# Kernel optimization log

Hardware: AMD Instinct MI355X
Metric: run time of the kernel (lower is better)

Reference implementation:

```python
import jax, jax.numpy as jnp
import numpy as np

NEG_SLOPE = 0.2  # PyG GATConv default negative_slope


def _gat(x, src, dst, N, W, a_src, a_dst, b, heads, ch, concat):
    # x: [N, F_in]; src/dst: [E] (self-loops already appended)
    h = (x @ W).reshape(N, heads, ch)                      # [N,H,C]
    s = jnp.sum(h * a_src, axis=-1)                        # [N,H]
    d = jnp.sum(h * a_dst, axis=-1)                        # [N,H]
    e = jax.nn.leaky_relu(s[src] + d[dst], NEG_SLOPE)      # [E,H]
    # segment softmax over incoming edges of each dst node
    m = jax.ops.segment_max(e, dst, num_segments=N)        # [N,H]
    ex = jnp.exp(e - m[dst])
    den = jax.ops.segment_sum(ex, dst, num_segments=N)     # [N,H]
    alpha = ex / den[dst]                                  # [E,H]
    out = jax.ops.segment_sum(h[src] * alpha[:, :, None], dst, num_segments=N)  # [N,H,C]
    out = out.reshape(N, heads * ch) if concat else out.mean(axis=1)
    return out + b


def setup_inputs() -> dict:
    key = jax.random.key(0)
    ks = jax.random.split(key, 20)
    N, E, F_in, H, C = 50000, 400000, 64, 4, 128
    x = jax.random.normal(ks[0], (N, F_in), dtype=jnp.float32)
    edge_index = jax.random.randint(ks[1], (2, E), 0, N, dtype=jnp.int64)

    def lin(k, fi, fo):
        return jax.random.normal(k, (fi, fo), dtype=jnp.float32) / np.float32(np.sqrt(fi))

    def att(k, h, c):
        return jax.random.normal(k, (h, c), dtype=jnp.float32) / np.float32(np.sqrt(c))

    return {
        "x": x, "edge_index": edge_index,
        "W1": lin(ks[2], F_in, H * C), "as1": att(ks[3], H, C), "ad1": att(ks[4], H, C), "b1": jnp.zeros((H * C,), jnp.float32),
        "W2": lin(ks[5], H * C, H * C), "as2": att(ks[6], H, C), "ad2": att(ks[7], H, C), "b2": jnp.zeros((H * C,), jnp.float32),
        "W3": lin(ks[8], H * C, C), "as3": att(ks[9], 1, C), "ad3": att(ks[10], 1, C), "b3": jnp.zeros((C,), jnp.float32),
        "cW1": lin(ks[11], C, C // 2), "cb1": jnp.zeros((C // 2,), jnp.float32),
        "cW2": lin(ks[12], C // 2, 2), "cb2": jnp.zeros((2,), jnp.float32),
    }


def reference(x, edge_index, W1, as1, ad1, b1, W2, as2, ad2, b2, W3, as3, ad3, b3, cW1, cb1, cW2, cb2):
    N = x.shape[0]
    loops = jnp.arange(N, dtype=edge_index.dtype)
    src = jnp.concatenate([edge_index[0], loops])
    dst = jnp.concatenate([edge_index[1], loops])
    h = _gat(x, src, dst, N, W1, as1, ad1, b1, 4, 128, True)
    h = jax.nn.relu(h)                         # dropout is identity at eval
    h = _gat(h, src, dst, N, W2, as2, ad2, b2, 4, 128, True)
    h = jax.nn.relu(h)
    h = _gat(h, src, dst, N, W3, as3, ad3, b3, 1, 128, False)
    out = jax.nn.relu(h @ cW1 + cb1) @ cW2 + cb2
    return jax.nn.log_softmax(out, axis=-1)
```

## Files before the change

kernel.cpp:

```cpp
#include <hip/hip_runtime.h>
#include <math.h>

#define NEG_SLOPE 0.2f

typedef __attribute__((ext_vector_type(8))) short short8;
typedef __attribute__((ext_vector_type(4))) float f32x4;
typedef unsigned short ushort_t;
typedef unsigned int u32;
typedef __attribute__((ext_vector_type(8))) unsigned short ushort8;
typedef __attribute__((ext_vector_type(4))) unsigned short ushort4v;

__device__ inline ushort_t f2bf(float f) {
    unsigned int u = __builtin_bit_cast(unsigned int, f);
    u += 0x7fffu + ((u >> 16) & 1u);
    return (ushort_t)(u >> 16);
}
__device__ inline float bf2f(ushort_t u) {
    unsigned int v = ((unsigned int)u) << 16;
    return __builtin_bit_cast(float, v);
}

__device__ inline void gl_lds16(const ushort_t* g, ushort_t* l) {
    __builtin_amdgcn_global_load_lds((const __attribute__((address_space(1))) u32*)g,
                                     (__attribute__((address_space(3))) u32*)l, 16, 0, 0);
}


__global__ void convert_count_kernel(const int* __restrict__ ei, int E, int N,
                                     int* __restrict__ deg,
                                     const float* __restrict__ x, ushort_t* __restrict__ xb, int n4x,
                                     const float* __restrict__ W1, ushort_t* __restrict__ W1t,
                                     const float* __restrict__ W2, ushort_t* __restrict__ W2t,
                                     const float* __restrict__ W3, ushort_t* __restrict__ W3t,
                                     const float* __restrict__ cW1, ushort_t* __restrict__ cW1t) {
    int i = blockIdx.x * blockDim.x + threadIdx.x;
    if (i < E + N) {
        int d = (i < E) ? ei[E + i] : (i - E);
        atomicAdd(&deg[d], 1);
    }
    if (i < n4x) {
        float4 v = ((const float4*)x)[i];
        ushort4v o;
        o.x = f2bf(v.x); o.y = f2bf(v.y); o.z = f2bf(v.z); o.w = f2bf(v.w);
        ((ushort4v*)xb)[i] = o;
        return;
    }
    int j = i - n4x;
    if (j < 64 * 512) {
        int k = j / 512, nn = j % 512;
        W1t[(size_t)nn * 64 + k] = f2bf(W1[j]);
        return;
    }
    j -= 64 * 512;
    if (j < 512 * 512) {
        int k = j / 512, nn = j % 512;
        W2t[(size_t)nn * 512 + k] = f2bf(W2[j]);
        return;
    }
    j -= 512 * 512;
    if (j < 512 * 128) {
        int k = j / 128, nn = j % 128;
        W3t[(size_t)nn * 512 + k] = f2bf(W3[j]);
        return;
    }
    j -= 512 * 128;
    if (j < 128 * 64) {
        int k = j / 64, nn = j % 64;
        cW1t[(size_t)nn * 128 + k] = f2bf(cW1[j]);
    }
}

__global__ void scan1_kernel(const int* __restrict__ deg, int* __restrict__ rowptr,
                             int* __restrict__ bsum, int N) {
    __shared__ int sdata[256];
    int t = threadIdx.x;
    int base = blockIdx.x * 1024 + t * 4;
    int v[4];
#pragma unroll
    for (int k = 0; k < 4; k++) v[k] = (base + k < N) ? deg[base + k] : 0;
    int s = v[0] + v[1] + v[2] + v[3];
    sdata[t] = s;
    __syncthreads();
    for (int off = 1; off < 256; off <<= 1) {
        int x = (t >= off) ? sdata[t - off] : 0;
        __syncthreads();
        sdata[t] += x;
        __syncthreads();
    }
    int p = sdata[t] - s;
    if (t == 255) bsum[blockIdx.x] = sdata[255];
#pragma unroll
    for (int k = 0; k < 4; k++) {
        if (base + k < N) rowptr[base + k] = p;
        p += v[k];
    }
}

__global__ void scan2_kernel(int* __restrict__ bsum, int* __restrict__ rowptr, int nb, int N) {
    __shared__ int sh[256];
    int t = threadIdx.x;
    int v = (t < nb) ? bsum[t] : 0;
    sh[t] = v;
    __syncthreads();
    for (int off = 1; off < 256; off <<= 1) {
        int x = (t >= off) ? sh[t - off] : 0;
        __syncthreads();
        sh[t] += x;
        __syncthreads();
    }
    if (t < nb) bsum[t] = sh[t] - v;
    if (t == 255) rowptr[N] = sh[255];
}

__global__ void scan3_kernel(const int* __restrict__ bsum, int* __restrict__ rowptr,
                             int* __restrict__ cursor, int N) {
    int i = blockIdx.x * blockDim.x + threadIdx.x;
    if (i < N) {
        int v = rowptr[i] + bsum[i >> 10];
        rowptr[i] = v;
        cursor[i] = v;
    }
}

__global__ void fill_csr_kernel(const int* __restrict__ ei, int E, int N,
                                int* __restrict__ cursor, int* __restrict__ srcS) {
    int e = blockIdx.x * blockDim.x + threadIdx.x;
    if (e >= E + N) return;
    int s, d;
    if (e < E) { s = ei[e]; d = ei[E + e]; }
    else       { s = e - E; d = e - E; }
    int pos = atomicAdd(&cursor[d], 1);
    srcS[pos] = s;
}


template <bool SCORES>
__global__ __launch_bounds__(256, 2) void gemm_bf16_kernel(
    const ushort_t* __restrict__ A, const ushort_t* __restrict__ Bt,
    ushort_t* __restrict__ C,
    const float* __restrict__ a_s, const float* __restrict__ a_d,
    float* __restrict__ sOut, float* __restrict__ dOut, int H,
    int M, int Ncols, int K) {
    __shared__ ushort_t As[128 * 32];
    __shared__ ushort_t Bs[128 * 32];
    __shared__ float sL[2][128];
    __shared__ float dL[2][128];
    int bm = blockIdx.y * 128, bn = blockIdx.x * 128;
    int tid = threadIdx.x;
    int w = tid >> 6, lane = tid & 63;
    int wy = w >> 1, wx = w & 1;
    int r = lane & 15, quad = lane >> 4;
    int srow = lane >> 2;
    int scol = (lane & 3) * 8;
    f32x4 acc[4][4] = {};
    for (int k0 = 0; k0 < K; k0 += 32) {
#pragma unroll
        for (int it = 0; it < 2; it++) {
            int rowb = w * 32 + it * 16;
            gl_lds16(A  + (size_t)(bm + rowb + srow) * K + k0 + scol, As + rowb * 32);
            gl_lds16(Bt + (size_t)(bn + rowb + srow) * K + k0 + scol, Bs + rowb * 32);
        }
        __syncthreads();
        short8 af[4], bfr[4];
#pragma unroll
        for (int i = 0; i < 4; i++)
            af[i] = *(const short8*)(As + (wy * 64 + i * 16 + r) * 32 + quad * 8);
#pragma unroll
        for (int j = 0; j < 4; j++)
            bfr[j] = *(const short8*)(Bs + (wx * 64 + j * 16 + r) * 32 + quad * 8);
#pragma unroll
        for (int i = 0; i < 4; i++)
#pragma unroll
            for (int j = 0; j < 4; j++)
                acc[i][j] = __builtin_amdgcn_mfma_f32_16x16x32_bf16(af[i], bfr[j], acc[i][j], 0, 0, 0);
        __syncthreads();
    }
#pragma unroll
    for (int i = 0; i < 4; i++) {
        int rowb = bm + wy * 64 + i * 16 + quad * 4;
#pragma unroll
        for (int j = 0; j < 4; j++) {
            int col = bn + wx * 64 + j * 16 + r;
            if (col >= Ncols) continue;
#pragma unroll
            for (int reg = 0; reg < 4; reg++) {
                int row = rowb + reg;
                if (row < M) C[(size_t)row * Ncols + col] = f2bf(acc[i][j][reg]);
            }
        }
    }
    if (SCORES) {
        int head = bn >> 7;
        float av[4], bv[4];
#pragma unroll
        for (int j = 0; j < 4; j++) {
            int c = wx * 64 + j * 16 + r;
            av[j] = a_s[head * 128 + c];
            bv[j] = a_d[head * 128 + c];
        }
#pragma unroll
        for (int i = 0; i < 4; i++) {
#pragma unroll
            for (int reg = 0; reg < 4; reg++) {
                float ps = acc[i][0][reg] * av[0] + acc[i][1][reg] * av[1]
                         + acc[i][2][reg] * av[2] + acc[i][3][reg] * av[3];
                float pd = acc[i][0][reg] * bv[0] + acc[i][1][reg] * bv[1]
                         + acc[i][2][reg] * bv[2] + acc[i][3][reg] * bv[3];
#pragma unroll
                for (int off = 8; off >= 1; off >>= 1) {
                    ps += __shfl_down(ps, off, 16);
                    pd += __shfl_down(pd, off, 16);
                }
                if (r == 0) {
                    int row128 = wy * 64 + i * 16 + quad * 4 + reg;
                    sL[wx][row128] = ps;
                    dL[wx][row128] = pd;
                }
            }
        }
        __syncthreads();
        if (tid < 128) {
            int row = bm + tid;
            if (row < M) {
                sOut[(size_t)row * H + head] = sL[0][tid] + sL[1][tid];
                dOut[(size_t)row * H + head] = dL[0][tid] + dL[1][tid];
            }
        }
    }
}


template <int HC, bool RELU>
__global__ void agg_fused_kernel(const ushort_t* __restrict__ h, const float* __restrict__ s,
                                 const float* __restrict__ dv, const int* __restrict__ rowptr,
                                 const int* __restrict__ srcS, const float* __restrict__ bias,
                                 ushort_t* __restrict__ outp, int N, int H) {
    const int TPN = HC / 8;
    const int NPB = 256 / TPN;
    int n = blockIdx.x * NPB + threadIdx.x / TPN;
    int c8 = threadIdx.x % TPN;
    if (n >= N) return;
    int head = (c8 * 8) >> 7;
    int g = c8 & 15;
    float dn = dv[(size_t)n * H + head];
    int beg = rowptr[n], end = rowptr[n + 1];
    float acc0[8] = {0.f, 0.f, 0.f, 0.f, 0.f, 0.f, 0.f, 0.f};
    float acc1[8] = {0.f, 0.f, 0.f, 0.f, 0.f, 0.f, 0.f, 0.f};
    float den = 0.f;
    for (int cb = beg; cb < end; cb += 16) {
        int je = cb + g;
        int svg = 0;
        float al = 0.f;
        if (je < end) {
            svg = srcS[je];
            float e = s[(size_t)svg * H + head] + dn;
            e = (e >= 0.f) ? e : NEG_SLOPE * e;
            al = expf(fminf(e, 80.f));
        }
        int kmax = end - cb;
        if (kmax > 16) kmax = 16;
        int k = 0;
        for (; k + 4 <= kmax; k += 4) {
            float a0 = __shfl(al, k, 16),     a1 = __shfl(al, k + 1, 16);
            float a2 = __shfl(al, k + 2, 16), a3 = __shfl(al, k + 3, 16);
            int s0 = __shfl(svg, k, 16),      s1 = __shfl(svg, k + 1, 16);
            int s2 = __shfl(svg, k + 2, 16),  s3 = __shfl(svg, k + 3, 16);
            den += a0 + a1 + a2 + a3;
            ushort8 hv0 = *(const ushort8*)(h + (size_t)s0 * HC + c8 * 8);
            ushort8 hv1 = *(const ushort8*)(h + (size_t)s1 * HC + c8 * 8);
            ushort8 hv2 = *(const ushort8*)(h + (size_t)s2 * HC + c8 * 8);
            ushort8 hv3 = *(const ushort8*)(h + (size_t)s3 * HC + c8 * 8);
#pragma unroll
            for (int kk = 0; kk < 8; kk++) {
                acc0[kk] += a0 * bf2f(hv0[kk]) + a2 * bf2f(hv2[kk]);
                acc1[kk] += a1 * bf2f(hv1[kk]) + a3 * bf2f(hv3[kk]);
            }
        }
        for (; k < kmax; k++) {
            float a0 = __shfl(al, k, 16);
            int s0 = __shfl(svg, k, 16);
            den += a0;
            ushort8 hv0 = *(const ushort8*)(h + (size_t)s0 * HC + c8 * 8);
#pragma unroll
            for (int kk = 0; kk < 8; kk++) acc0[kk] += a0 * bf2f(hv0[kk]);
        }
    }
    float inv = 1.f / den;
    float4 bv0 = ((const float4*)bias)[c8 * 2];
    float4 bv1 = ((const float4*)bias)[c8 * 2 + 1];
    float r[8];
#pragma unroll
    for (int k = 0; k < 8; k++) r[k] = (acc0[k] + acc1[k]) * inv;
    r[0] += bv0.x; r[1] += bv0.y; r[2] += bv0.z; r[3] += bv0.w;
    r[4] += bv1.x; r[5] += bv1.y; r[6] += bv1.z; r[7] += bv1.w;
    if (RELU) {
#pragma unroll
        for (int k = 0; k < 8; k++) r[k] = fmaxf(r[k], 0.f);
    }
    ushort8 o;
#pragma unroll
    for (int k = 0; k < 8; k++) o[k] = f2bf(r[k]);
    ((ushort8*)outp)[(size_t)n * TPN + c8] = o;
}


__global__ __launch_bounds__(256, 2) void cls_fused_kernel(
    const ushort_t* __restrict__ A, const ushort_t* __restrict__ Bt,
    const float* __restrict__ cb1, const float* __restrict__ cW2,
    const float* __restrict__ cb2, float* __restrict__ out, int M) {
    __shared__ ushort_t As[128 * 32];
    __shared__ ushort_t Bs[128 * 32];
    __shared__ float l0L[128];
    __shared__ float l1L[128];
    int bm = blockIdx.y * 128;
    int tid = threadIdx.x;
    int w = tid >> 6, lane = tid & 63;
    int wy = w >> 1, wx = w & 1;
    int r = lane & 15, quad = lane >> 4;
    int srow = lane >> 2;
    int scol = (lane & 3) * 8;
    const int K = 128;
    f32x4 acc[4][4] = {};
    for (int k0 = 0; k0 < K; k0 += 32) {
#pragma unroll
        for (int it = 0; it < 2; it++) {
            int rowb = w * 32 + it * 16;
            gl_lds16(A  + (size_t)(bm + rowb + srow) * K + k0 + scol, As + rowb * 32);
            gl_lds16(Bt + (size_t)(rowb + srow) * K + k0 + scol, Bs + rowb * 32);
        }
        __syncthreads();
        short8 af[4], bfr[4];
#pragma unroll
        for (int i = 0; i < 4; i++)
            af[i] = *(const short8*)(As + (wy * 64 + i * 16 + r) * 32 + quad * 8);
#pragma unroll
        for (int j = 0; j < 4; j++)
            bfr[j] = *(const short8*)(Bs + (wx * 64 + j * 16 + r) * 32 + quad * 8);
#pragma unroll
        for (int i = 0; i < 4; i++)
#pragma unroll
            for (int j = 0; j < 4; j++)
                acc[i][j] = __builtin_amdgcn_mfma_f32_16x16x32_bf16(af[i], bfr[j], acc[i][j], 0, 0, 0);
        __syncthreads();
    }
    if (wx == 0) {
        float c1v[4], w20[4], w21[4];
#pragma unroll
        for (int j = 0; j < 4; j++) {
            int c = j * 16 + r;
            c1v[j] = cb1[c];
            w20[j] = cW2[c * 2];
            w21[j] = cW2[c * 2 + 1];
        }
#pragma unroll
        for (int i = 0; i < 4; i++) {
#pragma unroll
            for (int reg = 0; reg < 4; reg++) {
                float ps = 0.f, pd = 0.f;
#pragma unroll
                for (int j = 0; j < 4; j++) {
                    float v = fmaxf(acc[i][j][reg] + c1v[j], 0.f);
                    ps += v * w20[j];
                    pd += v * w21[j];
                }
#pragma unroll
                for (int off = 8; off >= 1; off >>= 1) {
                    ps += __shfl_down(ps, off, 16);
                    pd += __shfl_down(pd, off, 16);
                }
                if (r == 0) {
                    int row128 = wy * 64 + i * 16 + quad * 4 + reg;
                    l0L[row128] = ps;
                    l1L[row128] = pd;
                }
            }
        }
    }
    __syncthreads();
    if (tid < 128) {
        int row = bm + tid;
        if (row < M) {
            float l0 = l0L[tid] + cb2[0];
            float l1 = l1L[tid] + cb2[1];
            float mm = fmaxf(l0, l1);
            float lse = mm + logf(expf(l0 - mm) + expf(l1 - mm));
            out[(size_t)row * 2 + 0] = l0 - lse;
            out[(size_t)row * 2 + 1] = l1 - lse;
        }
    }
}


extern "C" void kernel_launch(void* const* d_in, const int* in_sizes, int n_in,
                              void* d_out, int out_size, void* d_ws, size_t ws_size,
                              hipStream_t stream) {
    const float* x   = (const float*)d_in[0];
    const int*   ei  = (const int*)d_in[1];
    const float* W1  = (const float*)d_in[2];
    const float* as1 = (const float*)d_in[3];
    const float* ad1 = (const float*)d_in[4];
    const float* b1  = (const float*)d_in[5];
    const float* W2  = (const float*)d_in[6];
    const float* as2 = (const float*)d_in[7];
    const float* ad2 = (const float*)d_in[8];
    const float* b2  = (const float*)d_in[9];
    const float* W3  = (const float*)d_in[10];
    const float* as3 = (const float*)d_in[11];
    const float* ad3 = (const float*)d_in[12];
    const float* b3  = (const float*)d_in[13];
    const float* cW1 = (const float*)d_in[14];
    const float* cb1 = (const float*)d_in[15];
    const float* cW2 = (const float*)d_in[16];
    const float* cb2 = (const float*)d_in[17];
    float* outp = (float*)d_out;

    const int N  = in_sizes[0] / 64;
    const int E  = in_sizes[1] / 2;
    const int E2 = E + N;
    const int NB = (N + 1023) / 1024;
    const int n4x = N * 16;

    char* ws = (char*)d_ws;
    size_t off = 0;
    auto alloc = [&](size_t bytes) -> void* {
        void* p = ws + off;
        off += (bytes + 255) & ~(size_t)255;
        return p;
    };
    ushort_t* Ab     = (ushort_t*)alloc((size_t)N * 512 * 2);
    ushort_t* Bb     = (ushort_t*)alloc((size_t)N * 512 * 2);
    ushort_t* xb     = (ushort_t*)alloc((size_t)N * 64 * 2);
    ushort_t* W1t    = (ushort_t*)alloc((size_t)512 * 64 * 2);
    ushort_t* W2t    = (ushort_t*)alloc((size_t)512 * 512 * 2);
    ushort_t* W3t    = (ushort_t*)alloc((size_t)128 * 512 * 2);
    ushort_t* cW1t   = (ushort_t*)alloc((size_t)128 * 128 * 2);
    float*    sbuf   = (float*)alloc((size_t)N * 4 * 4);
    float*    dbuf   = (float*)alloc((size_t)N * 4 * 4);
    int*      srcS   = (int*)alloc((size_t)E2 * 4);
    int*      deg    = (int*)alloc((size_t)N * 4);
    int*      cursor = (int*)alloc((size_t)N * 4);
    int*      rowptr = (int*)alloc((size_t)(N + 1) * 4);
    int*      bsum   = (int*)alloc((size_t)256 * 4);
    (void)ws_size; (void)n_in; (void)out_size;

    hipMemsetAsync(deg, 0, (size_t)N * 4, stream);
    {
        int tot = n4x + 64 * 512 + 512 * 512 + 512 * 128 + 128 * 64;
        if (E2 > tot) tot = E2;
        convert_count_kernel<<<(tot + 255) / 256, 256, 0, stream>>>(
            ei, E, N, deg, x, xb, n4x, W1, W1t, W2, W2t, W3, W3t, cW1, cW1t);
    }
    scan1_kernel<<<NB, 256, 0, stream>>>(deg, rowptr, bsum, N);
    scan2_kernel<<<1, 256, 0, stream>>>(bsum, rowptr, NB, N);
    scan3_kernel<<<(N + 255) / 256, 256, 0, stream>>>(bsum, rowptr, cursor, N);
    fill_csr_kernel<<<(E2 + 255) / 256, 256, 0, stream>>>(ei, E, N, cursor, srcS);

    dim3 gB(256);
    dim3 g512(4, (N + 127) / 128);
    dim3 g128(1, (N + 127) / 128);

    gemm_bf16_kernel<true><<<g512, gB, 0, stream>>>(
        xb, W1t, Ab, as1, ad1, sbuf, dbuf, 4, N, 512, 64);
    agg_fused_kernel<512, true><<<(N + 3) / 4, 256, 0, stream>>>(
        Ab, sbuf, dbuf, rowptr, srcS, b1, Bb, N, 4);

    gemm_bf16_kernel<true><<<g512, gB, 0, stream>>>(
        Bb, W2t, Ab, as2, ad2, sbuf, dbuf, 4, N, 512, 512);
    agg_fused_kernel<512, true><<<(N + 3) / 4, 256, 0, stream>>>(
        Ab, sbuf, dbuf, rowptr, srcS, b2, Bb, N, 4);

    gemm_bf16_kernel<true><<<g128, gB, 0, stream>>>(
        Bb, W3t, Ab, as3, ad3, sbuf, dbuf, 1, N, 128, 512);
    agg_fused_kernel<128, false><<<(N + 15) / 16, 256, 0, stream>>>(
        Ab, sbuf, dbuf, rowptr, srcS, b3, Bb, N, 1);

    cls_fused_kernel<<<g128, gB, 0, stream>>>(Bb, cW1t, cb1, cW2, cb2, outp, N);
}
```

Measured before the change: 415.3 us.

## Software-pipeline gather loads and prefetch next edge chunk in GAT aggregation

Restructures the per-node aggregation loop so neighbor feature rows are loaded in double-buffered groups of four before the attention weights are computed. The source index and score for the next 16-edge chunk are prefetched during the current chunk's work. The goal is to hide the dependent-load latency chain (index, then score, then feature row) behind accumulation. In exchange it raises register pressure from eight buffered ushort8 rows plus prefetch state, which could lower occupancy.

```diff
diff --git a/kernel.cpp b/kernel.cpp
--- a/kernel.cpp
+++ b/kernel.cpp
@@ -247,44 +247,160 @@
     float acc0[8] = {0.f, 0.f, 0.f, 0.f, 0.f, 0.f, 0.f, 0.f};
     float acc1[8] = {0.f, 0.f, 0.f, 0.f, 0.f, 0.f, 0.f, 0.f};
     float den = 0.f;
+
+    const ushort_t* hb = h + (size_t)c8 * 8;
+
+    int je = beg + g;
+    int svg = 0;
+    float sv = 0.f;
+    if (je < end) {
+        svg = srcS[je];
+        sv = s[(size_t)svg * H + head];
+    }
+
     for (int cb = beg; cb < end; cb += 16) {
-        int je = cb + g;
-        int svg = 0;
+        int kmax = end - cb; if (kmax > 16) kmax = 16;
+        int svgc = svg;
+        float svc = sv;
+        ushort8 hA[4], hB[4];
+
+#pragma unroll
+        for (int q = 0; q < 4; q++) {
+            int sk = __shfl(svgc, q, 16);
+            if (q < kmax) hA[q] = *(const ushort8*)(hb + (size_t)sk * HC);
+        }
+        if (kmax > 4) {
+#pragma unroll
+            for (int q = 0; q < 4; q++) {
+                int sk = __shfl(svgc, 4 + q, 16);
+                if (4 + q < kmax) hB[q] = *(const ushort8*)(hb + (size_t)sk * HC);
+            }
+        }
+
+        int je2 = cb + 16 + g;
+        int svg_n = 0;
+        if (je2 < end) svg_n = srcS[je2];
+
         float al = 0.f;
-        if (je < end) {
-            svg = srcS[je];
-            float e = s[(size_t)svg * H + head] + dn;
+        if (g < kmax) {
+            float e = svc + dn;
             e = (e >= 0.f) ? e : NEG_SLOPE * e;
             al = expf(fminf(e, 80.f));
         }
-        int kmax = end - cb;
-        if (kmax > 16) kmax = 16;
-        int k = 0;
-        for (; k + 4 <= kmax; k += 4) {
-            float a0 = __shfl(al, k, 16),     a1 = __shfl(al, k + 1, 16);
-            float a2 = __shfl(al, k + 2, 16), a3 = __shfl(al, k + 3, 16);
-            int s0 = __shfl(svg, k, 16),      s1 = __shfl(svg, k + 1, 16);
-            int s2 = __shfl(svg, k + 2, 16),  s3 = __shfl(svg, k + 3, 16);
+
+        if (4 <= kmax) {
+            float a0 = __shfl(al, 0, 16), a1 = __shfl(al, 1, 16);
+            float a2 = __shfl(al, 2, 16), a3 = __shfl(al, 3, 16);
             den += a0 + a1 + a2 + a3;
-            ushort8 hv0 = *(const ushort8*)(h + (size_t)s0 * HC + c8 * 8);
-            ushort8 hv1 = *(const ushort8*)(h + (size_t)s1 * HC + c8 * 8);
-            ushort8 hv2 = *(const ushort8*)(h + (size_t)s2 * HC + c8 * 8);
-            ushort8 hv3 = *(const ushort8*)(h + (size_t)s3 * HC + c8 * 8);
 #pragma unroll
             for (int kk = 0; kk < 8; kk++) {
-                acc0[kk] += a0 * bf2f(hv0[kk]) + a2 * bf2f(hv2[kk]);
-                acc1[kk] += a1 * bf2f(hv1[kk]) + a3 * bf2f(hv3[kk]);
-            }
-        }
-        for (; k < kmax; k++) {
-            float a0 = __shfl(al, k, 16);
-            int s0 = __shfl(svg, k, 16);
-            den += a0;
-            ushort8 hv0 = *(const ushort8*)(h + (size_t)s0 * HC + c8 * 8);
-#pragma unroll
-            for (int kk = 0; kk < 8; kk++) acc0[kk] += a0 * bf2f(hv0[kk]);
-        }
-    }
+                acc0[kk] += a0 * bf2f(hA[0][kk]) + a2 * bf2f(hA[2][kk]);
+                acc1[kk] += a1 * bf2f(hA[1][kk]) + a3 * bf2f(hA[3][kk]);
+            }
+        } else {
+#pragma unroll
+            for (int q = 0; q < 4; q++) {
+                if (q < kmax) {
+                    float a = __shfl(al, q, 16);
+                    den += a;
+#pragma unroll
+                    for (int kk = 0; kk < 8; kk++) acc0[kk] += a * bf2f(hA[q][kk]);
+                }
+            }
+        }
+
+        if (kmax > 8) {
+#pragma unroll
+            for (int q = 0; q < 4; q++) {
+                int sk = __shfl(svgc, 8 + q, 16);
+                if (8 + q < kmax) hA[q] = *(const ushort8*)(hb + (size_t)sk * HC);
+            }
+        }
+
+        float sv_n = 0.f;
+        if (je2 < end) sv_n = s[(size_t)svg_n * H + head];
+
+        if (kmax > 4) {
+            if (8 <= kmax) {
+                float a0 = __shfl(al, 4, 16), a1 = __shfl(al, 5, 16);
+                float a2 = __shfl(al, 6, 16), a3 = __shfl(al, 7, 16);
+                den += a0 + a1 + a2 + a3;
+#pragma unroll
+                for (int kk = 0; kk < 8; kk++) {
+                    acc0[kk] += a0 * bf2f(hB[0][kk]) + a2 * bf2f(hB[2][kk]);
+                    acc1[kk] += a1 * bf2f(hB[1][kk]) + a3 * bf2f(hB[3][kk]);
+                }
+            } else {
+#pragma unroll
+                for (int q = 0; q < 4; q++) {
+                    if (4 + q < kmax) {
+                        float a = __shfl(al, 4 + q, 16);
+                        den += a;
+#pragma unroll
+                        for (int kk = 0; kk < 8; kk++) acc0[kk] += a * bf2f(hB[q][kk]);
+                    }
+                }
+            }
+        }
+
+        if (kmax > 12) {
+#pragma unroll
+            for (int q = 0; q < 4; q++) {
+                int sk = __shfl(svgc, 12 + q, 16);
+                if (12 + q < kmax) hB[q] = *(const ushort8*)(hb + (size_t)sk * HC);
+            }
+        }
+
+        if (kmax > 8) {
+            if (12 <= kmax) {
+                float a0 = __shfl(al, 8, 16), a1 = __shfl(al, 9, 16);
+                float a2 = __shfl(al, 10, 16), a3 = __shfl(al, 11, 16);
+                den += a0 + a1 + a2 + a3;
+#pragma unroll
+                for (int kk = 0; kk < 8; kk++) {
+                    acc0[kk] += a0 * bf2f(hA[0][kk]) + a2 * bf2f(hA[2][kk]);
+                    acc1[kk] += a1 * bf2f(hA[1][kk]) + a3 * bf2f(hA[3][kk]);
+                }
+            } else {
+#pragma unroll
+                for (int q = 0; q < 4; q++) {
+                    if (8 + q < kmax) {
+                        float a = __shfl(al, 8 + q, 16);
+                        den += a;
+#pragma unroll
+                        for (int kk = 0; kk < 8; kk++) acc0[kk] += a * bf2f(hA[q][kk]);
+                    }
+                }
+            }
+        }
+
+        if (kmax > 12) {
+            if (16 <= kmax) {
+                float a0 = __shfl(al, 12, 16), a1 = __shfl(al, 13, 16);
+                float a2 = __shfl(al, 14, 16), a3 = __shfl(al, 15, 16);
+                den += a0 + a1 + a2 + a3;
+#pragma unroll
+                for (int kk = 0; kk < 8; kk++) {
+                    acc0[kk] += a0 * bf2f(hB[0][kk]) + a2 * bf2f(hB[2][kk]);
+                    acc1[kk] += a1 * bf2f(hB[1][kk]) + a3 * bf2f(hB[3][kk]);
+                }
+            } else {
+#pragma unroll
+                for (int q = 0; q < 4; q++) {
+                    if (12 + q < kmax) {
+                        float a = __shfl(al, 12 + q, 16);
+                        den += a;
+#pragma unroll
+                        for (int kk = 0; kk < 8; kk++) acc0[kk] += a * bf2f(hB[q][kk]);
+                    }
+                }
+            }
+        }
+
+        svg = svg_n;
+        sv = sv_n;
+    }
+
     float inv = 1.f / den;
     float4 bv0 = ((const float4*)bias)[c8 * 2];
     float4 bv1 = ((const float4*)bias)[c8 * 2 + 1];
```

Measured after the change: 423.2 us. About the same (+1.9%).

## Reorder layer-1 GAT to aggregate raw features before linear projection

Applied to the files above, without the earlier changes.

For the first GAT layer, attention scores are computed directly from x using precomputed W1·a_src and W1·a_dst vectors. The 64-wide input features are aggregated per head before being multiplied by W1 in a per-head GEMM that also applies bias and ReLU. This halves the per-edge gather width and shrinks the layer-1 GEMM. The softmax drops max subtraction in favour of a clamp, and aggregated inputs are rounded to bf16, which may change numerics slightly.

```diff
diff --git a/kernel.cpp b/kernel.cpp
--- a/kernel.cpp
+++ b/kernel.cpp
@@ -32,7 +32,9 @@
                                      const float* __restrict__ W1, ushort_t* __restrict__ W1t,
                                      const float* __restrict__ W2, ushort_t* __restrict__ W2t,
                                      const float* __restrict__ W3, ushort_t* __restrict__ W3t,
-                                     const float* __restrict__ cW1, ushort_t* __restrict__ cW1t) {
+                                     const float* __restrict__ cW1, ushort_t* __restrict__ cW1t,
+                                     const float* __restrict__ as1, const float* __restrict__ ad1,
+                                     float* __restrict__ W1as, float* __restrict__ W1ad) {
     int i = blockIdx.x * blockDim.x + threadIdx.x;
     if (i < E + N) {
         int d = (i < E) ? ei[E + i] : (i - E);
@@ -67,6 +69,21 @@
     if (j < 128 * 64) {
         int k = j / 64, nn = j % 64;
         cW1t[(size_t)nn * 128 + k] = f2bf(cW1[j]);
+        return;
+    }
+    j -= 128 * 64;
+    if (j < 512) {
+        int k = j >> 3;
+        int idx = j & 7;
+        int h = idx & 3;
+        int sel = idx >> 2;
+        const float* av = sel ? ad1 : as1;
+        float* outw = sel ? W1ad : W1as;
+        const float* wrow = W1 + (size_t)k * 512 + h * 128;
+        const float* arow = av + h * 128;
+        float acc = 0.f;
+        for (int c = 0; c < 128; c++) acc += wrow[c] * arow[c];
+        outw[k * 4 + h] = acc;
     }
 }
 
@@ -131,6 +148,139 @@
     else       { s = e - E; d = e - E; }
     int pos = atomicAdd(&cursor[d], 1);
     srcS[pos] = s;
+}
+
+
+__global__ __launch_bounds__(256) void score1_kernel(const ushort_t* __restrict__ xb,
+                                                     const float* __restrict__ W1as,
+                                                     const float* __restrict__ W1ad,
+                                                     float* __restrict__ sOut,
+                                                     float* __restrict__ dOut, int N) {
+    __shared__ float wa[256];
+    __shared__ float wd[256];
+    int t = threadIdx.x;
+    wa[t] = W1as[t];
+    wd[t] = W1ad[t];
+    __syncthreads();
+    int n = blockIdx.x * 256 + t;
+    if (n >= N) return;
+    const ushort_t* xr = xb + (size_t)n * 64;
+    float s_[4] = {0.f, 0.f, 0.f, 0.f};
+    float d_[4] = {0.f, 0.f, 0.f, 0.f};
+#pragma unroll
+    for (int k8 = 0; k8 < 8; k8++) {
+        ushort8 xv = *(const ushort8*)(xr + k8 * 8);
+#pragma unroll
+        for (int kk = 0; kk < 8; kk++) {
+            float xf = bf2f(xv[kk]);
+            int k = k8 * 8 + kk;
+#pragma unroll
+            for (int h = 0; h < 4; h++) {
+                s_[h] += xf * wa[k * 4 + h];
+                d_[h] += xf * wd[k * 4 + h];
+            }
+        }
+    }
+#pragma unroll
+    for (int h = 0; h < 4; h++) {
+        sOut[(size_t)n * 4 + h] = s_[h];
+        dOut[(size_t)n * 4 + h] = d_[h];
+    }
+}
+
+
+__global__ void agg1x_kernel(const ushort_t* __restrict__ xb, const float* __restrict__ s,
+                             const float* __restrict__ dv, const int* __restrict__ rowptr,
+                             const int* __restrict__ srcS, ushort_t* __restrict__ outp, int N) {
+    int c = threadIdx.x & 31;
+    int slot = threadIdx.x >> 5;
+    int n = blockIdx.x * 8 + slot;
+    if (n >= N) return;
+    int h = c >> 3;
+    int d8 = c & 7;
+    float dn = dv[(size_t)n * 4 + h];
+    int beg = rowptr[n], end = rowptr[n + 1];
+    float acc[8] = {0.f, 0.f, 0.f, 0.f, 0.f, 0.f, 0.f, 0.f};
+    float den = 0.f;
+    for (int cb = beg; cb < end; cb += 8) {
+        int j = cb + d8;
+        int svg = 0;
+        float al = 0.f;
+        if (j < end) {
+            svg = srcS[j];
+            float e = s[(size_t)svg * 4 + h] + dn;
+            e = (e >= 0.f) ? e : NEG_SLOPE * e;
+            al = expf(fminf(e, 80.f));
+        }
+        int kmax = end - cb;
+        if (kmax > 8) kmax = 8;
+        for (int q = 0; q < kmax; q++) {
+            float a = __shfl(al, h * 8 + q, 32);
+            int sq = __shfl(svg, q, 32);
+            den += a;
+            ushort8 xv = *(const ushort8*)(xb + (size_t)sq * 64 + d8 * 8);
+#pragma unroll
+            for (int kk = 0; kk < 8; kk++) acc[kk] += a * bf2f(xv[kk]);
+        }
+    }
+    float inv = 1.f / den;
+    ushort8 o;
+#pragma unroll
+    for (int kk = 0; kk < 8; kk++) o[kk] = f2bf(acc[kk] * inv);
+    ((ushort8*)outp)[(size_t)n * 32 + c] = o;
+}
+
+
+__global__ __launch_bounds__(256, 2) void tgemm1_kernel(
+    const ushort_t* __restrict__ A, const ushort_t* __restrict__ Bt,
+    const float* __restrict__ bias, ushort_t* __restrict__ C, int M) {
+    __shared__ ushort_t As[128 * 32];
+    __shared__ ushort_t Bs[128 * 32];
+    int bm = blockIdx.y * 128, bn = blockIdx.x * 128;
+    int head = blockIdx.x;
+    int tid = threadIdx.x;
+    int w = tid >> 6, lane = tid & 63;
+    int wy = w >> 1, wx = w & 1;
+    int r = lane & 15, quad = lane >> 4;
+    int srow = lane >> 2;
+    int scol = (lane & 3) * 8;
+    f32x4 acc[4][4] = {};
+    for (int k0 = 0; k0 < 64; k0 += 32) {
+#pragma unroll
+        for (int it = 0; it < 2; it++) {
+            int rowb = w * 32 + it * 16;
+            gl_lds16(A  + (size_t)(bm + rowb + srow) * 256 + head * 64 + k0 + scol, As + rowb * 32);
+            gl_lds16(Bt + (size_t)(bn + rowb + srow) * 64 + k0 + scol, Bs + rowb * 32);
+        }
+        __syncthreads();
+        short8 af[4], bfr[4];
+#pragma unroll
+        for (int i = 0; i < 4; i++)
+            af[i] = *(const short8*)(As + (wy * 64 + i * 16 + r) * 32 + quad * 8);
+#pragma unroll
+        for (int j = 0; j < 4; j++)
+            bfr[j] = *(const short8*)(Bs + (wx * 64 + j * 16 + r) * 32 + quad * 8);
+#pragma unroll
+        for (int i = 0; i < 4; i++)
+#pragma unroll
+            for (int j = 0; j < 4; j++)
+                acc[i][j] = __builtin_amdgcn_mfma_f32_16x16x32_bf16(af[i], bfr[j], acc[i][j], 0, 0, 0);
+        __syncthreads();
+    }
+#pragma unroll
+    for (int i = 0; i < 4; i++) {
+        int rowb = bm + wy * 64 + i * 16 + quad * 4;
+#pragma unroll
+        for (int j = 0; j < 4; j++) {
+            int col = bn + wx * 64 + j * 16 + r;
+            float bv = bias[col];
+#pragma unroll
+            for (int reg = 0; reg < 4; reg++) {
+                int row = rowb + reg;
+                if (row < M) C[(size_t)row * 512 + col] = f2bf(fmaxf(acc[i][j][reg] + bv, 0.f));
+            }
+        }
+    }
 }
 
 
@@ -434,6 +584,8 @@
     ushort_t* W2t    = (ushort_t*)alloc((size_t)512 * 512 * 2);
     ushort_t* W3t    = (ushort_t*)alloc((size_t)128 * 512 * 2);
     ushort_t* cW1t   = (ushort_t*)alloc((size_t)128 * 128 * 2);
+    float*    W1as   = (float*)alloc((size_t)64 * 4 * 4);
+    float*    W1ad   = (float*)alloc((size_t)64 * 4 * 4);
     float*    sbuf   = (float*)alloc((size_t)N * 4 * 4);
     float*    dbuf   = (float*)alloc((size_t)N * 4 * 4);
     int*      srcS   = (int*)alloc((size_t)E2 * 4);
@@ -445,10 +597,11 @@
 
     hipMemsetAsync(deg, 0, (size_t)N * 4, stream);
     {
-        int tot = n4x + 64 * 512 + 512 * 512 + 512 * 128 + 128 * 64;
+        int tot = n4x + 64 * 512 + 512 * 512 + 512 * 128 + 128 * 64 + 512;
         if (E2 > tot) tot = E2;
         convert_count_kernel<<<(tot + 255) / 256, 256, 0, stream>>>(
-            ei, E, N, deg, x, xb, n4x, W1, W1t, W2, W2t, W3, W3t, cW1, cW1t);
+            ei, E, N, deg, x, xb, n4x, W1, W1t, W2, W2t, W3, W3t, cW1, cW1t,
+            as1, ad1, W1as, W1ad);
     }
     scan1_kernel<<<NB, 256, 0, stream>>>(deg, rowptr, bsum, N);
     scan2_kernel<<<1, 256, 0, stream>>>(bsum, rowptr, NB, N);
@@ -459,10 +612,9 @@
     dim3 g512(4, (N + 127) / 128);
     dim3 g128(1, (N + 127) / 128);
 
-    gemm_bf16_kernel<true><<<g512, gB, 0, stream>>>(
-        xb, W1t, Ab, as1, ad1, sbuf, dbuf, 4, N, 512, 64);
-    agg_fused_kernel<512, true><<<(N + 3) / 4, 256, 0, stream>>>(
-        Ab, sbuf, dbuf, rowptr, srcS, b1, Bb, N, 4);
+    score1_kernel<<<(N + 255) / 256, 256, 0, stream>>>(xb, W1as, W1ad, sbuf, dbuf, N);
+    agg1x_kernel<<<(N + 7) / 8, 256, 0, stream>>>(xb, sbuf, dbuf, rowptr, srcS, Ab, N);
+    tgemm1_kernel<<<g512, gB, 0, stream>>>(Ab, W1t, b1, Bb, N);
 
     gemm_bf16_kernel<true><<<g512, gB, 0, stream>>>(
         Bb, W2t, Ab, as2, ad2, sbuf, dbuf, 4, N, 512, 512);
```

New measurement: 382.2 us. -8.0%, faster.
